# Kernel optimization log

Hardware: AMD Instinct MI355X
Metric: run time of the kernel (lower is better)

The kernel has to match this reference:

```python
import jax, jax.numpy as jnp
import numpy as np

jax.config.update("jax_enable_x64", True)  # torch uses double for the scale decomposition

ACC = 23  # 'accuracy' in integer_multiply_shift_round


def _fixed_point_mul(x_int, new_scale):
    """Bit-exact integer multiply-shift-round: x * new_scale where
    new_scale = m * 2**e (frexp), m quantized to ACC-bit integer mantissa."""
    m, e = jnp.frexp(new_scale)                      # m in [0.5, 1)
    nm = jnp.round(m * (1 << ACC)).astype(jnp.int64)  # torch casts to int32 (ACC<32); int64 is a safe superset
    tmp = x_int.astype(jnp.int64) * nm                # [B,S,D] int64
    e = e.astype(jnp.int64)
    sl = jnp.maximum(e - ACC, 0)                      # left-shift amount (e - ACC >= 0 branch)
    sr = jnp.maximum(ACC - e, 0)                      # right-shift amount (sr_round_na branch)
    left = tmp << sl
    bit = (tmp < 0).astype(jnp.int64)
    nudge = (jnp.int64(1) << jnp.maximum(sr - 1, 0)) - bit   # round-half-away-from-zero nudge
    right = jnp.where(sr > 0, (tmp + nudge) >> sr, tmp)      # sr==0 -> identity (sr_round_na early return)
    return jnp.where(e - ACC >= 0, left, right)


def setup_inputs() -> dict:
    key = jax.random.key(0)
    k1, k2 = jax.random.split(key)
    B, S, D = 4, 4096, 2048
    # integer-valued pre-activations (int32 accumulators), stored as float32 holding exact ints
    x = jax.random.randint(k1, (B, S, D), -2048, 2048, dtype=jnp.int32).astype(jnp.float32)
    identity = jax.random.randint(k2, (B, S, D), -2048, 2048, dtype=jnp.int32).astype(jnp.float32)
    return {
        "x": x,
        "identity": identity,
        "pre_act_scaling_factor": jnp.array([0.004], jnp.float32),
        "identity_scaling_factor": jnp.array([0.002], jnp.float32),
        "x_min": jnp.array([-8.0], jnp.float32),   # calibrated activation range buffers
        "x_max": jnp.array([8.0], jnp.float32),
    }


def reference(x, identity, pre_act_scaling_factor, identity_scaling_factor, x_min, x_max):
    bit = 8
    n = 2 ** (bit - 1) - 1  # 127
    # symmetric_linear_quantization_params (per-tensor)
    scale = jnp.clip(jnp.maximum(jnp.abs(x_min), jnp.abs(x_max)), 1e-8, None) / n  # [1] float32
    # FixedPointMul: requantize pre_act and identity to the output scale, add, clamp
    s64 = scale.astype(jnp.float64)
    ns_x = pre_act_scaling_factor.astype(jnp.float64) / s64
    ns_id = identity_scaling_factor.astype(jnp.float64) / s64
    out = _fixed_point_mul(x.astype(jnp.int64), ns_x) + _fixed_point_mul(identity.astype(jnp.int64), ns_id)
    q = jnp.clip(out, -n - 1, n).astype(jnp.int8)  # bit_num<=8 -> int8
    # QuantAct returns dequantized activation and its scale
    return q.astype(jnp.float32) * scale.astype(jnp.float32), scale
```

## Files before the change

### kernel.cpp

```cpp
#include <hip/hip_runtime.h>
#include <math.h>

#define ACC_BITS 23

struct QParams {
    float scale;
    int   fast;
    int   nmx_hi, nmx_lo, Kx, srx12;
    int   nmi_hi, nmi_lo, Ki, sri12;
    long long nm_x64, nm_i64;
    int   e_x, e_i;
};

__global__ void qparams_kernel(const float* __restrict__ pre_sf,
                               const float* __restrict__ id_sf,
                               const float* __restrict__ xminp,
                               const float* __restrict__ xmaxp,
                               QParams* __restrict__ p,
                               float* __restrict__ out_scale)
{
    float s = fmaxf(fmaxf(fabsf(xminp[0]), fabsf(xmaxp[0])), 1e-8f);
    float scale = s / 127.0f;

    double s64  = (double)scale;
    double ns_x = (double)pre_sf[0] / s64;
    double ns_i = (double)id_sf[0] / s64;

    int e_x, e_i;
    double m_x = frexp(ns_x, &e_x);
    double m_i = frexp(ns_i, &e_i);
    long long nm_x = (long long)rint(m_x * 8388608.0);
    long long nm_i = (long long)rint(m_i * 8388608.0);

    p->scale  = scale;
    p->nm_x64 = nm_x;  p->e_x = e_x;
    p->nm_i64 = nm_i;  p->e_i = e_i;

    long long ax = nm_x, ai = nm_i;
    int ex = e_x, ei = e_i;
    if (ax == (1LL << 23)) { ax >>= 1; ex += 1; }
    if (ai == (1LL << 23)) { ai >>= 1; ei += 1; }
    int sr_x = ACC_BITS - ex, sr_i = ACC_BITS - ei;

    int fast = (ax > 0) && (ax < (1LL << 23)) &&
               (ai > 0) && (ai < (1LL << 23)) &&
               (sr_x >= 12) && (sr_x <= 30) && (sr_i >= 12) && (sr_i <= 30);
    p->fast = fast;
    p->nmx_hi = (int)(ax >> 12); p->nmx_lo = (int)(ax & 0xFFF);
    p->nmi_hi = (int)(ai >> 12); p->nmi_lo = (int)(ai & 0xFFF);
    p->Kx = fast ? (1 << (sr_x - 1)) : 0;
    p->Ki = fast ? (1 << (sr_i - 1)) : 0;
    p->srx12 = sr_x - 12;
    p->sri12 = sr_i - 12;

    *out_scale = scale;
}

__device__ __forceinline__ long long fixed_point_mul64(long long xi, long long nm, int e) {
    long long tmp = xi * nm;
    if (e - ACC_BITS >= 0) {
        return tmp << (e - ACC_BITS);
    } else {
        int sr = ACC_BITS - e;
        long long nudge = (1LL << (sr - 1)) - (long long)(tmp < 0);
        return (tmp + nudge) >> sr;
    }
}

__device__ __forceinline__ int fpm24(int xi, int nm_hi, int nm_lo, int K, int sr12) {
    int bit = (int)((unsigned)xi >> 31);
    int B = (__mul24(xi, nm_lo) + K - bit) >> 12;
    int A = __mul24(xi, nm_hi);
    return (A + B) >> sr12;
}

typedef float f32x4 __attribute__((ext_vector_type(4)));

#define TPB   256
#define VPT   4
#define TILE  (TPB * VPT)

__global__ void __launch_bounds__(TPB)
quantact_main(const f32x4* __restrict__ x,
              const f32x4* __restrict__ idn,
              f32x4* __restrict__ out,
              const QParams* __restrict__ p,
              int n4, int n)
{
    const float scale = p->scale;
    const int base = blockIdx.x * TILE + threadIdx.x;

    if (p->fast) {
        const int nmx_hi = p->nmx_hi, nmx_lo = p->nmx_lo, Kx = p->Kx, srx = p->srx12;
        const int nmi_hi = p->nmi_hi, nmi_lo = p->nmi_lo, Ki = p->Ki, sri = p->sri12;

        if (base + (VPT - 1) * TPB < n4) {
            f32x4 xv[VPT], iv[VPT];
            #pragma unroll
            for (int k = 0; k < VPT; ++k) xv[k] = x[base + k * TPB];
            #pragma unroll
            for (int k = 0; k < VPT; ++k) iv[k] = idn[base + k * TPB];

            f32x4 ov[VPT];
            #pragma unroll
            for (int k = 0; k < VPT; ++k) {
                #pragma unroll
                for (int c = 0; c < 4; ++c) {
                    int o = fpm24((int)xv[k][c], nmx_hi, nmx_lo, Kx, srx)
                          + fpm24((int)iv[k][c], nmi_hi, nmi_lo, Ki, sri);
                    o = o < -128 ? -128 : (o > 127 ? 127 : o);
                    ov[k][c] = (float)o * scale;
                }
            }
            #pragma unroll
            for (int k = 0; k < VPT; ++k) out[base + k * TPB] = ov[k];
        } else {
            #pragma unroll
            for (int k = 0; k < VPT; ++k) {
                int i = base + k * TPB;
                if (i < n4) {
                    f32x4 xv = x[i], iv = idn[i], ov;
                    #pragma unroll
                    for (int c = 0; c < 4; ++c) {
                        int o = fpm24((int)xv[c], nmx_hi, nmx_lo, Kx, srx)
                              + fpm24((int)iv[c], nmi_hi, nmi_lo, Ki, sri);
                        o = o < -128 ? -128 : (o > 127 ? 127 : o);
                        ov[c] = (float)o * scale;
                    }
                    out[i] = ov;
                }
            }
        }
    } else {
        const long long nm64_x = p->nm_x64, nm64_i = p->nm_i64;
        const int e_x = p->e_x, e_i = p->e_i;
        #pragma unroll
        for (int k = 0; k < VPT; ++k) {
            int i = base + k * TPB;
            if (i < n4) {
                f32x4 xv = x[i], iv = idn[i], ov;
                #pragma unroll
                for (int c = 0; c < 4; ++c) {
                    long long o = fixed_point_mul64((long long)xv[c], nm64_x, e_x)
                                + fixed_point_mul64((long long)iv[c], nm64_i, e_i);
                    o = o < -128 ? -128 : (o > 127 ? 127 : o);
                    ov[c] = (float)(int)o * scale;
                }
                out[i] = ov;
            }
        }
    }

    if (blockIdx.x == 0) {
        const float* xs  = (const float*)x;
        const float* is_ = (const float*)idn;
        float* os = (float*)out;
        const long long nm64_x = p->nm_x64, nm64_i = p->nm_i64;
        const int e_x = p->e_x, e_i = p->e_i;
        for (int j = n4 * 4 + (int)threadIdx.x; j < n; j += TPB) {
            long long o = fixed_point_mul64((long long)xs[j], nm64_x, e_x)
                        + fixed_point_mul64((long long)is_[j], nm64_i, e_i);
            o = o < -128 ? -128 : (o > 127 ? 127 : o);
            os[j] = (float)(int)o * scale;
        }
    }
}

extern "C" void kernel_launch(void* const* d_in, const int* in_sizes, int n_in,
                              void* d_out, int out_size, void* d_ws, size_t ws_size,
                              hipStream_t stream) {
    const f32x4* x      = (const f32x4*)d_in[0];
    const f32x4* idn    = (const f32x4*)d_in[1];
    const float* pre_sf = (const float*)d_in[2];
    const float* id_sf  = (const float*)d_in[3];
    const float* xmin   = (const float*)d_in[4];
    const float* xmax   = (const float*)d_in[5];

    int n  = in_sizes[0];
    int n4 = n / 4;

    float* out       = (float*)d_out;
    float* out_scale = out + n;
    QParams* p       = (QParams*)d_ws;

    qparams_kernel<<<1, 1, 0, stream>>>(pre_sf, id_sf, xmin, xmax, p, out_scale);

    int grid = (n4 + TILE - 1) / TILE;
    if (grid < 1) grid = 1;
    quantact_main<<<grid, TPB, 0, stream>>>(x, idn, (f32x4*)out, p, n4, n);
}
```

Baseline: 318.2 us.

## Use persistent grid-stride blocks with double-buffered register prefetch

Replaces the one-tile-per-block launch with a fixed grid of up to 2048 persistent blocks that stride over tiles. Each block alternates between two register buffers, loading the next tile while computing and storing the current one. The slow 64-bit path also becomes a grid-stride loop, and a leftover-tile loop handles the remainder. This aims to cut block scheduling overhead and overlap memory latency with compute, at the cost of more registers and possibly lower occupancy.

```diff
diff --git a/kernel.cpp b/kernel.cpp
--- a/kernel.cpp
+++ b/kernel.cpp
@@ -77,67 +77,73 @@
 typedef float f32x4 __attribute__((ext_vector_type(4)));
 
 #define TPB   256
-#define VPT   4
-#define TILE  (TPB * VPT)
+#define VPT   2
+#define TILEV (TPB * VPT)
 
 __global__ void __launch_bounds__(TPB)
 quantact_main(const f32x4* __restrict__ x,
               const f32x4* __restrict__ idn,
               f32x4* __restrict__ out,
               const QParams* __restrict__ p,
-              int n4, int n)
+              int n4, int n, int tiles)
 {
     const float scale = p->scale;
-    const int base = blockIdx.x * TILE + threadIdx.x;
+    const int tid = threadIdx.x;
+    const int G = gridDim.x;
 
     if (p->fast) {
         const int nmx_hi = p->nmx_hi, nmx_lo = p->nmx_lo, Kx = p->Kx, srx = p->srx12;
         const int nmi_hi = p->nmi_hi, nmi_lo = p->nmi_lo, Ki = p->Ki, sri = p->sri12;
 
-        if (base + (VPT - 1) * TPB < n4) {
-            f32x4 xv[VPT], iv[VPT];
+        f32x4 xa0, xa1, ia0, ia1;
+        f32x4 xb0, xb1, ib0, ib1;
+
+        auto LOADA = [&](int j) {
+            int b = j * TILEV + tid;
+            xa0 = x[b]; xa1 = x[b + TPB]; ia0 = idn[b]; ia1 = idn[b + TPB];
+        };
+        auto LOADB = [&](int j) {
+            int b = j * TILEV + tid;
+            xb0 = x[b]; xb1 = x[b + TPB]; ib0 = idn[b]; ib1 = idn[b + TPB];
+        };
+        auto CS = [&](int j, f32x4& xv0, f32x4& iv0, f32x4& xv1, f32x4& iv1) {
+            int b = j * TILEV + tid;
+            f32x4 o0, o1;
             #pragma unroll
-            for (int k = 0; k < VPT; ++k) xv[k] = x[base + k * TPB];
-            #pragma unroll
-            for (int k = 0; k < VPT; ++k) iv[k] = idn[base + k * TPB];
-
-            f32x4 ov[VPT];
-            #pragma unroll
-            for (int k = 0; k < VPT; ++k) {
-                #pragma unroll
-                for (int c = 0; c < 4; ++c) {
-                    int o = fpm24((int)xv[k][c], nmx_hi, nmx_lo, Kx, srx)
-                          + fpm24((int)iv[k][c], nmi_hi, nmi_lo, Ki, sri);
-                    o = o < -128 ? -128 : (o > 127 ? 127 : o);
-                    ov[k][c] = (float)o * scale;
-                }
-            }
-            #pragma unroll
-            for (int k = 0; k < VPT; ++k) out[base + k * TPB] = ov[k];
-        } else {
-            #pragma unroll
-            for (int k = 0; k < VPT; ++k) {
-                int i = base + k * TPB;
-                if (i < n4) {
-                    f32x4 xv = x[i], iv = idn[i], ov;
-                    #pragma unroll
-                    for (int c = 0; c < 4; ++c) {
-                        int o = fpm24((int)xv[c], nmx_hi, nmx_lo, Kx, srx)
-                              + fpm24((int)iv[c], nmi_hi, nmi_lo, Ki, sri);
-                        o = o < -128 ? -128 : (o > 127 ? 127 : o);
-                        ov[c] = (float)o * scale;
-                    }
-                    out[i] = ov;
-                }
-            }
-        }
-    } else {
-        const long long nm64_x = p->nm_x64, nm64_i = p->nm_i64;
-        const int e_x = p->e_x, e_i = p->e_i;
-        #pragma unroll
-        for (int k = 0; k < VPT; ++k) {
-            int i = base + k * TPB;
-            if (i < n4) {
+            for (int c = 0; c < 4; ++c) {
+                int q0 = fpm24((int)xv0[c], nmx_hi, nmx_lo, Kx, srx)
+                       + fpm24((int)iv0[c], nmi_hi, nmi_lo, Ki, sri);
+                q0 = q0 < -128 ? -128 : (q0 > 127 ? 127 : q0);
+                o0[c] = (float)q0 * scale;
+                int q1 = fpm24((int)xv1[c], nmx_hi, nmx_lo, Kx, srx)
+                       + fpm24((int)iv1[c], nmi_hi, nmi_lo, Ki, sri);
+                q1 = q1 < -128 ? -128 : (q1 > 127 ? 127 : q1);
+                o1[c] = (float)q1 * scale;
+            }
+            out[b] = o0;
+            out[b + TPB] = o1;
+        };
+
+        int j = blockIdx.x;
+        if (j < tiles) {
+            LOADA(j);
+            for (;;) {
+                int j2 = j + G;
+                if (j2 >= tiles) { CS(j, xa0, ia0, xa1, ia1); break; }
+                LOADB(j2);
+                CS(j, xa0, ia0, xa1, ia1);
+                int j3 = j2 + G;
+                if (j3 >= tiles) { CS(j2, xb0, ib0, xb1, ib1); break; }
+                LOADA(j3);
+                CS(j2, xb0, ib0, xb1, ib1);
+                j = j3;
+            }
+        }
+
+        if (blockIdx.x == 0) {
+            const long long nm64_x = p->nm_x64, nm64_i = p->nm_i64;
+            const int e_x = p->e_x, e_i = p->e_i;
+            for (int i = tiles * TILEV + tid; i < n4; i += TPB) {
                 f32x4 xv = x[i], iv = idn[i], ov;
                 #pragma unroll
                 for (int c = 0; c < 4; ++c) {
@@ -149,6 +155,20 @@
                 out[i] = ov;
             }
         }
+    } else {
+        const long long nm64_x = p->nm_x64, nm64_i = p->nm_i64;
+        const int e_x = p->e_x, e_i = p->e_i;
+        for (int i = blockIdx.x * TPB + tid; i < n4; i += G * TPB) {
+            f32x4 xv = x[i], iv = idn[i], ov;
+            #pragma unroll
+            for (int c = 0; c < 4; ++c) {
+                long long o = fixed_point_mul64((long long)xv[c], nm64_x, e_x)
+                            + fixed_point_mul64((long long)iv[c], nm64_i, e_i);
+                o = o < -128 ? -128 : (o > 127 ? 127 : o);
+                ov[c] = (float)(int)o * scale;
+            }
+            out[i] = ov;
+        }
     }
 
     if (blockIdx.x == 0) {
@@ -157,11 +177,11 @@
         float* os = (float*)out;
         const long long nm64_x = p->nm_x64, nm64_i = p->nm_i64;
         const int e_x = p->e_x, e_i = p->e_i;
-        for (int j = n4 * 4 + (int)threadIdx.x; j < n; j += TPB) {
-            long long o = fixed_point_mul64((long long)xs[j], nm64_x, e_x)
-                        + fixed_point_mul64((long long)is_[j], nm64_i, e_i);
+        for (int j2 = n4 * 4 + tid; j2 < n; j2 += TPB) {
+            long long o = fixed_point_mul64((long long)xs[j2], nm64_x, e_x)
+                        + fixed_point_mul64((long long)is_[j2], nm64_i, e_i);
             o = o < -128 ? -128 : (o > 127 ? 127 : o);
-            os[j] = (float)(int)o * scale;
+            os[j2] = (float)(int)o * scale;
         }
     }
 }
@@ -178,6 +198,7 @@
 
     int n  = in_sizes[0];
     int n4 = n / 4;
+    int tiles = n4 / TILEV;
 
     float* out       = (float*)d_out;
     float* out_scale = out + n;
@@ -185,7 +206,8 @@
 
     qparams_kernel<<<1, 1, 0, stream>>>(pre_sf, id_sf, xmin, xmax, p, out_scale);
 
-    int grid = (n4 + TILE - 1) / TILE;
+    int grid = 2048;
+    if (tiles > 0 && tiles < grid) grid = tiles;
     if (grid < 1) grid = 1;
-    quantact_main<<<grid, TPB, 0, stream>>>(x, idn, (f32x4*)out, p, n4, n);
-}
+    quantact_main<<<grid, TPB, 0, stream>>>(x, idn, (f32x4*)out, p, n4, n, tiles);
+}
```

Result: slower. 324.7 us (+2.0%).
